# Kernel tuning notes

Measured on AMD Instinct MI355X. Metric: run time of the kernel, lower is better.

## Reference

```python
import jax, jax.numpy as jnp
import numpy as np

D = 384      # d_model
DM = 256     # memory feature dim
DF = 1536    # dim_feedforward
EPS = 1e-5


def _layer_norm(x, g, b):
    m = jnp.mean(x, axis=-1, keepdims=True)
    v = jnp.mean(jnp.square(x - m), axis=-1, keepdims=True)
    return (x - m) * jax.lax.rsqrt(v + EPS) * g + b


def setup_inputs() -> dict:
    key = jax.random.key(0)
    ks = jax.random.split(key, 24)
    B, T, T1, Tc = 8, 2048, 2048, 2048
    s = 0.02
    inp = {
        "tgt": jax.random.normal(ks[0], (B, T, D), jnp.float32),
        "memory": jax.random.normal(ks[1], (B, T1, DM), jnp.float32),
        "a1": jnp.float32(0.5),
        "score_c": jax.random.normal(ks[2], (B, 1, Tc, T1), jnp.float32) * 0.1,
        "out_c": jax.random.normal(ks[3], (B, Tc, D), jnp.float32),
        # attention projections
        "Wq": jax.random.normal(ks[4], (D, D), jnp.float32) * s,
        "bq": jnp.zeros((D,), jnp.float32),
        "Wk": jax.random.normal(ks[5], (DM, D), jnp.float32) * s,
        "bk": jnp.zeros((D,), jnp.float32),
        "Wv": jax.random.normal(ks[6], (DM, D), jnp.float32) * s,
        "bv": jnp.zeros((D,), jnp.float32),
        "Wu": jax.random.normal(ks[7], (D, D), jnp.float32) * s,  # unknown
        "bu": jnp.zeros((D,), jnp.float32),
        "Wn": jax.random.normal(ks[8], (D, D), jnp.float32) * s,  # known
        "bn": jnp.zeros((D,), jnp.float32),
        # FFN
        "W1": jax.random.normal(ks[9], (D, DF), jnp.float32) * s,
        "b1": jnp.zeros((DF,), jnp.float32),
        "W2": jax.random.normal(ks[10], (DF, D), jnp.float32) * s,
        "b2": jnp.zeros((D,), jnp.float32),
        # LayerNorms
        "g1": jnp.ones((D,), jnp.float32),
        "be1": jnp.zeros((D,), jnp.float32),
        "g2": jnp.ones((D,), jnp.float32),
        "be2": jnp.zeros((D,), jnp.float32),
    }
    return inp


def reference(tgt, memory, a1, score_c, out_c,
              Wq, bq, Wk, bk, Wv, bv, Wu, bu, Wn, bn,
              W1, b1, W2, b2, g1, be1, g2, be2):
    # --- En_De_Attention (n_head = 1; dropout p=0 / eval mode -> identity) ---
    scale = 1.0 / jnp.sqrt(jnp.float32(D))
    q = tgt @ Wq + bq                  # [B,T,D]
    k = memory @ Wk + bk               # [B,T1,D]
    v = memory @ Wv + bv               # [B,T1,D]
    att = jnp.einsum('btd,bsd->bts', q, k) * scale            # [B,T,T1]

    unknow = tgt @ Wu + bu             # [B,T,D]
    know = out_c @ Wn + bn             # [B,Tc,D]
    score1 = jnp.einsum('btd,bcd->btc', unknow, know) * scale  # [B,T,Tc]
    mixed = jnp.einsum('btc,bcs->bts', score1, score_c[:, 0])  # [B,T,T1]

    # tt = a1 in (0,1]: blended-score branch of the original module
    score = a1 * jax.nn.softmax(mixed, axis=-1) \
          + (1.0 - a1) * jax.nn.softmax(att, axis=-1)          # [B,T,T1]
    z = jnp.einsum('bts,bsd->btd', score, v)                   # [B,T,D]

    # --- residual + norm1 ---
    x = _layer_norm(tgt + z, g1, be1)
    # --- FFN (relu) + residual + norm2 (dropout eval -> identity) ---
    ff = jax.nn.relu(x @ W1 + b1) @ W2 + b2
    out = _layer_norm(x + ff, g2, be2)
    # score2 returned with head dim, matching torch shape [B,1,T,T1]
    return out, score[:, None]
```

## Files before the change

kernel.cpp:

```cpp
#include <hip/hip_runtime.h>
#include <stdint.h>

typedef __attribute__((ext_vector_type(8))) short bf16x8;
typedef __attribute__((ext_vector_type(4))) float f32x4;

__device__ __forceinline__ short f2bf(float f) {
    union { float f; unsigned u; } v; v.f = f;
    unsigned r = v.u + 0x7fffu + ((v.u >> 16) & 1u);
    return (short)(r >> 16);
}
__device__ __forceinline__ float bf2f(short s) {
    union { unsigned u; float f; } v;
    v.u = ((unsigned)(unsigned short)s) << 16;
    return v.f;
}

__device__ __forceinline__ void gld16(const void* g, void* l) {
    auto gp = reinterpret_cast<const __attribute__((address_space(1))) unsigned int*>(
        reinterpret_cast<uintptr_t>(g));
    auto lp = reinterpret_cast<__attribute__((address_space(3))) unsigned int*>(
        reinterpret_cast<uintptr_t>(l));
    __builtin_amdgcn_global_load_lds(gp, lp, 16, 0, 0);
}

template<int OUTBF, int BIASMODE , int DORELU>
__global__ __launch_bounds__(256, 2) void gemmWide(
    const short* __restrict__ Ag, const short* __restrict__ Bg,
    void* __restrict__ Cg, const float* __restrict__ bias,
    int K, int lda, int ldb, int ldc,
    long long sA, long long sB, long long sC,
    long long dA, long long dB, long long dC, float scale)
{
    __shared__ short lds[3 * 12288];
    const int t = threadIdx.x;
    const int lane = t & 63;
    const int wave = t >> 6;
    const int wm = wave >> 1, wn = wave & 1;

    const int gx = gridDim.x, gy = gridDim.y;
    const int nwg = gx * gy * gridDim.z;
    int id = blockIdx.x + gx * (blockIdx.y + gy * blockIdx.z);
    id = (id & 7) * (nwg >> 3) + (id >> 3);
    const int bx = id % gx;
    const int by = (id / gx) % gy;
    const int bz = id / (gx * gy);
    const int zlo = bz & 7, zhi = bz >> 3;

    const long long row0 = (long long)by * 128;
    const long long col0 = (long long)bx * 256;
    const int NT = K >> 5;

    const int gk = ((t & 3) ^ ((t >> 2) & 3) ^ ((t >> 4) & 3)) * 8;
    const short* Asrc = Ag + zlo * sA + zhi * dA + (row0 + (t >> 2)) * (long long)lda + gk;
    const short* Bsrc = Bg + zlo * sB + zhi * dB + (col0 + (t >> 2)) * (long long)ldb + gk;

    const int frow = lane & 15;
    const int fcol = ((lane >> 4) ^ (frow & 3) ^ ((frow >> 2) & 3)) * 8;

    f32x4 acc[4][8] = {};

#define STG(BUF, KC) do { \
        gld16(Asrc + (KC), &lds[(BUF) * 12288 + t * 8]); \
        gld16(Asrc + (KC) + 64LL * lda, &lds[(BUF) * 12288 + 2048 + t * 8]); \
        gld16(Bsrc + (KC), &lds[(BUF) * 12288 + 4096 + t * 8]); \
        gld16(Bsrc + (KC) + 64LL * ldb, &lds[(BUF) * 12288 + 6144 + t * 8]); \
        gld16(Bsrc + (KC) + 128LL * ldb, &lds[(BUF) * 12288 + 8192 + t * 8]); \
        gld16(Bsrc + (KC) + 192LL * ldb, &lds[(BUF) * 12288 + 10240 + t * 8]); } while (0)

    STG(0, 0);
    STG(1, 32);
    asm volatile("s_waitcnt vmcnt(6)\ns_barrier" ::: "memory");

    for (int kt = 0; kt < NT; ++kt) {
        const int rb = (kt % 3) * 12288;
        bf16x8 av[4], bv[8];
#pragma unroll
        for (int m = 0; m < 4; ++m)
            av[m] = *(const bf16x8*)&lds[rb + (wm * 64 + m * 16 + frow) * 32 + fcol];
#pragma unroll
        for (int n = 0; n < 8; ++n)
            bv[n] = *(const bf16x8*)&lds[rb + 4096 + (wn * 128 + n * 16 + frow) * 32 + fcol];
        if (kt + 2 < NT) STG((kt + 2) % 3, (long long)(kt + 2) * 32);
        __builtin_amdgcn_s_setprio(1);
#pragma unroll
        for (int m = 0; m < 4; ++m)
#pragma unroll
            for (int n = 0; n < 8; ++n)
                acc[m][n] = __builtin_amdgcn_mfma_f32_16x16x32_bf16(av[m], bv[n], acc[m][n], 0, 0, 0);
        __builtin_amdgcn_s_setprio(0);
        if (kt + 1 < NT) {
            if (kt + 2 < NT) asm volatile("s_waitcnt vmcnt(6)\ns_barrier" ::: "memory");
            else             asm volatile("s_waitcnt vmcnt(0)\ns_barrier" ::: "memory");
        }
    }
#undef STG

    const int crow = (lane >> 4) * 4;
    const int ccol = lane & 15;
    const long long cz = zlo * sC + zhi * dC;
#pragma unroll
    for (int m = 0; m < 4; ++m)
#pragma unroll
        for (int n = 0; n < 8; ++n)
#pragma unroll
            for (int i = 0; i < 4; ++i) {
                long long r = row0 + wm * 64 + m * 16 + crow + i;
                long long c = col0 + wn * 128 + n * 16 + ccol;
                float v = acc[m][n][i] * scale;
                if (BIASMODE == 1) v += bias[c];
                if (DORELU) v = fmaxf(v, 0.0f);
                long long idx = cz + r * (long long)ldc + c;
                if (OUTBF) ((short*)Cg)[idx] = f2bf(v);
                else ((float*)Cg)[idx] = v;
            }
}

template<int OUTBF, int BIASMODE , int DORELU>
__global__ __launch_bounds__(256, 3) void gemm128r(
    const short* __restrict__ Ag, const short* __restrict__ Bg,
    void* __restrict__ Cg, const float* __restrict__ bias,
    int K, int lda, int ldb, int ldc,
    long long sA, long long sB, long long sC,
    long long dA, long long dB, long long dC, float scale)
{
    __shared__ short lds[3 * 8192];
    const int t = threadIdx.x;
    const int lane = t & 63;
    const int wave = t >> 6;
    const int wm = wave >> 1, wn = wave & 1;

    const int gx = gridDim.x, gy = gridDim.y;
    const int nwg = gx * gy * gridDim.z;
    int id = blockIdx.x + gx * (blockIdx.y + gy * blockIdx.z);
    id = (id & 7) * (nwg >> 3) + (id >> 3);
    const int bx = id % gx;
    const int by = (id / gx) % gy;
    const int bz = id / (gx * gy);
    const int zlo = bz & 7, zhi = bz >> 3;

    const long long row0 = (long long)by * 128;
    const long long col0 = (long long)bx * 128;
    const int NT = K >> 5;

    const int gk = ((t & 3) ^ ((t >> 2) & 3) ^ ((t >> 4) & 3)) * 8;
    const short* Asrc = Ag + zlo * sA + zhi * dA + (row0 + (t >> 2)) * (long long)lda + gk;
    const short* Bsrc = Bg + zlo * sB + zhi * dB + (col0 + (t >> 2)) * (long long)ldb + gk;

    const int frow = lane & 15;
    const int fcol = ((lane >> 4) ^ (frow & 3) ^ ((frow >> 2) & 3)) * 8;

    f32x4 acc[4][4] = {};

#define STG(BUF, KC) do { \
        gld16(Asrc + (KC), &lds[(BUF) * 8192 + t * 8]); \
        gld16(Asrc + (KC) + 64LL * lda, &lds[(BUF) * 8192 + 2048 + t * 8]); \
        gld16(Bsrc + (KC), &lds[(BUF) * 8192 + 4096 + t * 8]); \
        gld16(Bsrc + (KC) + 64LL * ldb, &lds[(BUF) * 8192 + 6144 + t * 8]); } while (0)

    STG(0, 0);
    STG(1, 32);
    asm volatile("s_waitcnt vmcnt(4)\ns_barrier" ::: "memory");

    for (int kt = 0; kt < NT; ++kt) {
        const int rb = (kt % 3) * 8192;
        bf16x8 av[4], bv[4];
#pragma unroll
        for (int m = 0; m < 4; ++m)
            av[m] = *(const bf16x8*)&lds[rb + (wm * 64 + m * 16 + frow) * 32 + fcol];
#pragma unroll
        for (int n = 0; n < 4; ++n)
            bv[n] = *(const bf16x8*)&lds[rb + 4096 + (wn * 64 + n * 16 + frow) * 32 + fcol];
        if (kt + 2 < NT) STG((kt + 2) % 3, (long long)(kt + 2) * 32);
        __builtin_amdgcn_s_setprio(1);
#pragma unroll
        for (int m = 0; m < 4; ++m)
#pragma unroll
            for (int n = 0; n < 4; ++n)
                acc[m][n] = __builtin_amdgcn_mfma_f32_16x16x32_bf16(av[m], bv[n], acc[m][n], 0, 0, 0);
        __builtin_amdgcn_s_setprio(0);
        if (kt + 1 < NT) {
            if (kt + 2 < NT) asm volatile("s_waitcnt vmcnt(4)\ns_barrier" ::: "memory");
            else             asm volatile("s_waitcnt vmcnt(0)\ns_barrier" ::: "memory");
        }
    }
#undef STG

    const int crow = (lane >> 4) * 4;
    const int ccol = lane & 15;
    const long long cz = zlo * sC + zhi * dC;
#pragma unroll
    for (int m = 0; m < 4; ++m)
#pragma unroll
        for (int n = 0; n < 4; ++n)
#pragma unroll
            for (int i = 0; i < 4; ++i) {
                long long r = row0 + wm * 64 + m * 16 + crow + i;
                long long c = col0 + wn * 64 + n * 16 + ccol;
                float v = acc[m][n][i] * scale;
                if (BIASMODE == 1) v += bias[c];
                if (BIASMODE == 2) v += bias[r];
                if (DORELU) v = fmaxf(v, 0.0f);
                long long idx = cz + r * (long long)ldc + c;
                if (OUTBF) ((short*)Cg)[idx] = f2bf(v);
                else ((float*)Cg)[idx] = v;
            }
}

__global__ __launch_bounds__(256, 3) void gemm128rr(
    const short* __restrict__ A1, const short* __restrict__ B1,
    short* __restrict__ C1, const float* __restrict__ bias1,
    int K1, int lda1, int ldb1, int ldc1,
    const short* __restrict__ A2, const short* __restrict__ B2,
    short* __restrict__ C2, const float* __restrict__ bias2,
    int K2, int lda2, int ldb2, int ldc2)
{
    __shared__ short lds[3 * 8192];
    const int t = threadIdx.x;
    const int lane = t & 63;
    const int wave = t >> 6;
    const int wm = wave >> 1, wn = wave & 1;

    const int gx = gridDim.x, gy = gridDim.y;
    const int nwg = gx * gy;
    int id = blockIdx.x + gx * blockIdx.y;
    id = (id & 7) * (nwg >> 3) + (id >> 3);
    const int bx = id % gx;
    const int by = id / gx;

    const bool sel = bx >= 6;
    const int bxx = sel ? bx - 6 : bx;
    const short* Ag = sel ? A2 : A1;
    const short* Bg = sel ? B2 : B1;
    short* Cg = sel ? C2 : C1;
    const float* bias = sel ? bias2 : bias1;
    const int K = sel ? K2 : K1;
    const int lda = sel ? lda2 : lda1;
    const int ldb = sel ? ldb2 : ldb1;
    const int ldc = sel ? ldc2 : ldc1;

    const long long row0 = (long long)by * 128;
    const long long col0 = (long long)bxx * 128;
    const int NT = K >> 5;

    const int gk = ((t & 3) ^ ((t >> 2) & 3) ^ ((t >> 4) & 3)) * 8;
    const short* Asrc = Ag + (row0 + (t >> 2)) * (long long)lda + gk;
    const short* Bsrc = Bg + (col0 + (t >> 2)) * (long long)ldb + gk;

    const int frow = lane & 15;
    const int fcol = ((lane >> 4) ^ (frow & 3) ^ ((frow >> 2) & 3)) * 8;

    f32x4 acc[4][4] = {};

#define STG(BUF, KC) do { \
        gld16(Asrc + (KC), &lds[(BUF) * 8192 + t * 8]); \
        gld16(Asrc + (KC) + 64LL * lda, &lds[(BUF) * 8192 + 2048 + t * 8]); \
        gld16(Bsrc + (KC), &lds[(BUF) * 8192 + 4096 + t * 8]); \
        gld16(Bsrc + (KC) + 64LL * ldb, &lds[(BUF) * 8192 + 6144 + t * 8]); } while (0)

    STG(0, 0);
    STG(1, 32);
    asm volatile("s_waitcnt vmcnt(4)\ns_barrier" ::: "memory");

    for (int kt = 0; kt < NT; ++kt) {
        const int rb = (kt % 3) * 8192;
        bf16x8 av[4], bv[4];
#pragma unroll
        for (int m = 0; m < 4; ++m)
            av[m] = *(const bf16x8*)&lds[rb + (wm * 64 + m * 16 + frow) * 32 + fcol];
#pragma unroll
        for (int n = 0; n < 4; ++n)
            bv[n] = *(const bf16x8*)&lds[rb + 4096 + (wn * 64 + n * 16 + frow) * 32 + fcol];
        if (kt + 2 < NT) STG((kt + 2) % 3, (long long)(kt + 2) * 32);
        __builtin_amdgcn_s_setprio(1);
#pragma unroll
        for (int m = 0; m < 4; ++m)
#pragma unroll
            for (int n = 0; n < 4; ++n)
                acc[m][n] = __builtin_amdgcn_mfma_f32_16x16x32_bf16(av[m], bv[n], acc[m][n], 0, 0, 0);
        __builtin_amdgcn_s_setprio(0);
        if (kt + 1 < NT) {
            if (kt + 2 < NT) asm volatile("s_waitcnt vmcnt(4)\ns_barrier" ::: "memory");
            else             asm volatile("s_waitcnt vmcnt(0)\ns_barrier" ::: "memory");
        }
    }
#undef STG

    const int crow = (lane >> 4) * 4;
    const int ccol = lane & 15;
#pragma unroll
    for (int m = 0; m < 4; ++m)
#pragma unroll
        for (int n = 0; n < 4; ++n)
#pragma unroll
            for (int i = 0; i < 4; ++i) {
                long long r = row0 + wm * 64 + m * 16 + crow + i;
                long long c = col0 + wn * 64 + n * 16 + ccol;
                float v = acc[m][n][i] + bias[c];
                Cg[r * (long long)ldc + c] = f2bf(v);
            }
}

#define RD_A(RB, M, KS) (*(const bf16x8*)&lds[(RB) + (wm * 64 + (M) * 16 + frow) * 64 + \
        ((((KS) << 2) | fq) ^ (frow & 7)) * 8])
#define RD_B(RB, Nn, KS) (*(const bf16x8*)&lds[(RB) + 8192 + (wn * 64 + (Nn) * 16 + frow) * 64 + \
        ((((KS) << 2) | fq) ^ (frow & 7)) * 8])

__global__ __launch_bounds__(256, 2) void gemm128pz(
    const short* __restrict__ A1, const short* __restrict__ B1, short* __restrict__ C1,
    const float* __restrict__ bias1, int K1, int lda1, int ldb1, int ldc1,
    long long sB1, long long sC1,
    const short* __restrict__ A2, const short* __restrict__ B2, short* __restrict__ C2,
    const float* __restrict__ bias2, int K2, int lda2, int ldb2, int ldc2,
    long long sB2, long long sC2)
{
    __shared__ short lds[2 * 16384];
    const int t = threadIdx.x;
    const int lane = t & 63;
    const int wave = t >> 6;
    const int wm = wave >> 1, wn = wave & 1;

    const int gx = gridDim.x, gy = gridDim.y;
    const int nwg = gx * gy * gridDim.z;
    int id = blockIdx.x + gx * (blockIdx.y + gy * blockIdx.z);
    id = (id & 7) * (nwg >> 3) + (id >> 3);
    const int bx = id % gx;
    const int by = (id / gx) % gy;
    const int bz = id / (gx * gy);

    const bool sel = bz >= 8;
    const int zz = bz & 7;
    const short* Ag = sel ? A2 : A1;
    const short* Bg = sel ? B2 : B1;
    short* Cg = sel ? C2 : C1;
    const float* bias = sel ? bias2 : bias1;
    const int K = sel ? K2 : K1;
    const int lda = sel ? lda2 : lda1;
    const int ldb = sel ? ldb2 : ldb1;
    const int ldc = sel ? ldc2 : ldc1;
    const long long sB = sel ? sB2 : sB1;
    const long long sC = sel ? sC2 : sC1;

    const long long row0 = (long long)by * 128;
    const long long col0 = (long long)bx * 128;
    const int NT = K >> 6;

    const int srow = t >> 3;
    const int gk = ((t & 7) ^ (srow & 7)) * 8;
    const short* Asrc = Ag + (row0 + srow) * (long long)lda + gk;
    const short* Bsrc = Bg + (long long)zz * sB + (col0 + srow) * (long long)ldb + gk;

    const int frow = lane & 15;
    const int fq = lane >> 4;

    f32x4 acc[4][4] = {};

#define STAGE_A(WB, KC) do { _Pragma("unroll") \
        for (int r = 0; r < 4; ++r) \
            gld16(Asrc + (KC) + (long long)r * 32 * lda, &lds[(WB) + t * 8 + r * 2048]); } while (0)
#define STAGE_B(WB, KC) do { _Pragma("unroll") \
        for (int r = 0; r < 4; ++r) \
            gld16(Bsrc + (KC) + (long long)r * 32 * ldb, &lds[(WB) + 8192 + t * 8 + r * 2048]); } while (0)

    STAGE_A(0, 0);
    STAGE_B(0, 0);
    asm volatile("s_waitcnt vmcnt(0)\ns_barrier" ::: "memory");

    for (int kt = 0; kt < NT; ++kt) {
        const int rb = (kt & 1) << 14;
        const int wb = ((kt + 1) & 1) << 14;
        const bool st = (kt + 1) < NT;
        const long long kc = (long long)(kt + 1) << 6;

        bf16x8 av[4], bv[4];

#pragma unroll
        for (int m = 0; m < 4; ++m) av[m] = RD_A(rb, m, 0);
#pragma unroll
        for (int n = 0; n < 4; ++n) bv[n] = RD_B(rb, n, 0);
        if (st) STAGE_A(wb, kc);
        asm volatile("s_barrier" ::: "memory");
        __builtin_amdgcn_s_setprio(1);
#pragma unroll
        for (int m = 0; m < 4; ++m)
#pragma unroll
            for (int n = 0; n < 4; ++n)
                acc[m][n] = __builtin_amdgcn_mfma_f32_16x16x32_bf16(av[m], bv[n], acc[m][n], 0, 0, 0);
        __builtin_amdgcn_s_setprio(0);
        asm volatile("s_barrier" ::: "memory");

#pragma unroll
        for (int m = 0; m < 4; ++m) av[m] = RD_A(rb, m, 1);
#pragma unroll
        for (int n = 0; n < 4; ++n) bv[n] = RD_B(rb, n, 1);
        if (st) STAGE_B(wb, kc);
        asm volatile("s_barrier" ::: "memory");
        __builtin_amdgcn_s_setprio(1);
#pragma unroll
        for (int m = 0; m < 4; ++m)
#pragma unroll
            for (int n = 0; n < 4; ++n)
                acc[m][n] = __builtin_amdgcn_mfma_f32_16x16x32_bf16(av[m], bv[n], acc[m][n], 0, 0, 0);
        __builtin_amdgcn_s_setprio(0);
        if (st) asm volatile("s_waitcnt vmcnt(0)\ns_barrier" ::: "memory");
        else    asm volatile("s_barrier" ::: "memory");
    }
#undef STAGE_A
#undef STAGE_B

    const int crow = (lane >> 4) * 4;
    const int ccol = lane & 15;
    const long long cz = (long long)zz * sC;
#pragma unroll
    for (int m = 0; m < 4; ++m)
#pragma unroll
        for (int n = 0; n < 4; ++n)
#pragma unroll
            for (int i = 0; i < 4; ++i) {
                long long r = row0 + wm * 64 + m * 16 + crow + i;
                long long c = col0 + wn * 64 + n * 16 + ccol;
                float v = acc[m][n][i] + bias[r];
                Cg[cz + r * (long long)ldc + c] = f2bf(v);
            }
}
#undef RD_A
#undef RD_B

__global__ __launch_bounds__(256) void prologue(
    const float* __restrict__ tgt, const float* __restrict__ mem, const float* __restrict__ outc,
    const float* __restrict__ bq, const float* __restrict__ bu,
    short* __restrict__ tgtb, short* __restrict__ memb, short* __restrict__ outcb,
    float* __restrict__ qubias,
    const float* __restrict__ Wq, const float* __restrict__ Wk, const float* __restrict__ Wv,
    const float* __restrict__ Wu, const float* __restrict__ Wn,
    const float* __restrict__ W1, const float* __restrict__ W2,
    short* __restrict__ WquT, short* __restrict__ WkT, short* __restrict__ WvT,
    short* __restrict__ WnT, short* __restrict__ W1T, short* __restrict__ W2T,
    const float* __restrict__ score_c, short* __restrict__ scoreCt)
{
    __shared__ __align__(16) char smem[33792];
    const int blk = blockIdx.x;
    const int t = threadIdx.x;

    if (blk < 4096) {
        const long long R1 = 1572864;
        const long long R2 = R1 + 1048576;
        const long long base = (long long)blk * 1024 + t;
#pragma unroll
        for (int s = 0; s < 4; ++s) {
            long long i = base + s * 256;
            const float* in; short* out; long long j;
            if (i < R1) { in = tgt; out = tgtb; j = i; }
            else if (i < R2) { in = mem; out = memb; j = i - R1; }
            else { in = outc; out = outcb; j = i - R2; }
            float4 v = ((const float4*)in)[j];
            short4 o;
            o.x = f2bf(v.x); o.y = f2bf(v.y); o.z = f2bf(v.z); o.w = f2bf(v.w);
            ((short4*)out)[j] = o;
        }
        return;
    }

    if (blk == 4096) {
        if (t < 192)
            ((float4*)qubias)[t] = (t < 96) ? ((const float4*)bq)[t] : ((const float4*)bu)[t - 96];
        return;
    }

    if (blk < 4541) {
        float (*tile)[65] = (float(*)[65])smem;
        int b = blk - 4097;
        const float* in; short* out; int R, C, local;
        if (b < 36)       { in = Wq; out = WquT;          R = 384;  C = 384;  local = b; }
        else if (b < 60)  { in = Wk; out = WkT;           R = 256;  C = 384;  local = b - 36; }
        else if (b < 84)  { in = Wv; out = WvT;           R = 256;  C = 384;  local = b - 60; }
        else if (b < 120) { in = Wu; out = WquT + 147456; R = 384;  C = 384;  local = b - 84; }
        else if (b < 156) { in = Wn; out = WnT;           R = 384;  C = 384;  local = b - 120; }
        else if (b < 300) { in = W1; out = W1T;           R = 384;  C = 1536; local = b - 156; }
        else              { in = W2; out = W2T;           R = 1536; C = 384;  local = b - 300; }
        const int nbx = C >> 6;
        const int r0 = (local / nbx) * 64, c0 = (local % nbx) * 64;
        const int lr = t >> 6, lc = t & 63;
#pragma unroll
        for (int i = 0; i < 16; ++i) {
            int r = lr * 16 + i;
            tile[r][lc] = in[(long long)(r0 + r) * C + c0 + lc];
        }
        __syncthreads();
#pragma unroll
        for (int i = 0; i < 16; ++i) {
            int r = lr * 16 + i;
            out[(long long)(c0 + r) * R + r0 + lc] = f2bf(tile[lc][r]);
        }
        return;
    }

    {
        short (*stile)[264] = (short(*)[264])smem;
        const long long S2 = 2048LL * 2048;
        int local = blk - 4541;
        const int ct = local & 7;
        const int rt = (local >> 3) & 31;
        const int bz = local >> 8;
        const long long zoff = (long long)bz * S2;
        const int r0 = rt * 64, c0 = ct * 256;

        const int tr = t >> 2;
        const int tc = t & 3;
        const float* src = score_c + zoff + (long long)(r0 + tr) * 2048 + c0 + tc * 64;
#pragma unroll
        for (int i = 0; i < 16; ++i) {
            float4 v = ((const float4*)src)[i];
            short4 o;
            o.x = f2bf(v.x); o.y = f2bf(v.y); o.z = f2bf(v.z); o.w = f2bf(v.w);
            *(short4*)&stile[tr][tc * 64 + i * 4] = o;
        }
        __syncthreads();
        short* dst = scoreCt + zoff + (long long)(c0 + t) * 2048 + r0;
#pragma unroll
        for (int rr = 0; rr < 16; ++rr) {
            short4 o;
            o.x = stile[4 * rr + 0][t];
            o.y = stile[4 * rr + 1][t];
            o.z = stile[4 * rr + 2][t];
            o.w = stile[4 * rr + 3][t];
            ((short4*)dst)[rr] = o;
        }
    }
}

__global__ __launch_bounds__(256) void softmax_blend(
    const short* __restrict__ attb, const short* __restrict__ mixb,
    const float* __restrict__ a1p,
    float* __restrict__ outF, short* __restrict__ outB)
{
    const int S = 2048;
    const long long row = blockIdx.x;
    const short* ar = attb + row * S;
    const short* mr = mixb + row * S;
    const int t = threadIdx.x;
    const int wave = t >> 6;

    bf16x8 a8 = *(const bf16x8*)&ar[t * 8];
    bf16x8 m8 = *(const bf16x8*)&mr[t * 8];
    float av[8], mv[8];
#pragma unroll
    for (int i = 0; i < 8; ++i) { av[i] = bf2f(a8[i]); mv[i] = bf2f(m8[i]); }

    float amax = av[0], mmax = mv[0];
#pragma unroll
    for (int i = 1; i < 8; ++i) { amax = fmaxf(amax, av[i]); mmax = fmaxf(mmax, mv[i]); }
#pragma unroll
    for (int o = 32; o; o >>= 1) {
        amax = fmaxf(amax, __shfl_xor(amax, o));
        mmax = fmaxf(mmax, __shfl_xor(mmax, o));
    }
    __shared__ float red[2][4];
    if ((t & 63) == 0) { red[0][wave] = amax; red[1][wave] = mmax; }
    __syncthreads();
    amax = fmaxf(fmaxf(red[0][0], red[0][1]), fmaxf(red[0][2], red[0][3]));
    mmax = fmaxf(fmaxf(red[1][0], red[1][1]), fmaxf(red[1][2], red[1][3]));

    float asum = 0.f, msum = 0.f;
#pragma unroll
    for (int i = 0; i < 8; ++i) {
        av[i] = __expf(av[i] - amax); asum += av[i];
        mv[i] = __expf(mv[i] - mmax); msum += mv[i];
    }
#pragma unroll
    for (int o = 32; o; o >>= 1) {
        asum += __shfl_xor(asum, o);
        msum += __shfl_xor(msum, o);
    }
    __shared__ float red2[2][4];
    if ((t & 63) == 0) { red2[0][wave] = asum; red2[1][wave] = msum; }
    __syncthreads();
    asum = red2[0][0] + red2[0][1] + red2[0][2] + red2[0][3];
    msum = red2[1][0] + red2[1][1] + red2[1][2] + red2[1][3];

    const float a1 = a1p[0];
    const float wm = a1 / msum;
    const float wa = (1.0f - a1) / asum;

    float o0[8];
    bf16x8 ob;
#pragma unroll
    for (int i = 0; i < 8; ++i) {
        float s = wm * mv[i] + wa * av[i];
        o0[i] = s;
        ob[i] = f2bf(s);
    }
    float4 f0, f1;
    f0.x = o0[0]; f0.y = o0[1]; f0.z = o0[2]; f0.w = o0[3];
    f1.x = o0[4]; f1.y = o0[5]; f1.z = o0[6]; f1.w = o0[7];
    *(float4*)&outF[row * S + t * 8] = f0;
    *(float4*)&outF[row * S + t * 8 + 4] = f1;
    *(bf16x8*)&outB[row * S + t * 8] = ob;
}

template<int WRITE_F, int WRITE_BF, int TWO_Y, int XBF>
__global__ __launch_bounds__(256) void ln_kernel(
    const void* __restrict__ Xv, const float* __restrict__ Yr,
    const float* __restrict__ Y2,
    const float* __restrict__ g, const float* __restrict__ be,
    float* __restrict__ outF, short* __restrict__ outB)
{
    const int Dm = 384;
    const int wave = threadIdx.x >> 6, lane = threadIdx.x & 63;
    const long long row = (long long)blockIdx.x * 4 + wave;
    const float* y = Yr + row * Dm;
    const float* y2 = TWO_Y ? (Y2 + row * Dm) : nullptr;
    float h[6];
    float s = 0.f, s2 = 0.f;
#pragma unroll
    for (int j = 0; j < 6; ++j) {
        int c = j * 64 + lane;
        float xv;
        if (XBF) xv = bf2f(((const short*)Xv)[row * Dm + c]);
        else     xv = ((const float*)Xv)[row * Dm + c];
        h[j] = xv + y[c];
        if (TWO_Y) h[j] += y2[c];
        s += h[j]; s2 += h[j] * h[j];
    }
#pragma unroll
    for (int o = 32; o; o >>= 1) { s += __shfl_xor(s, o); s2 += __shfl_xor(s2, o); }
    const float mean = s * (1.0f / 384.0f);
    const float var = s2 * (1.0f / 384.0f) - mean * mean;
    const float rstd = rsqrtf(var + 1e-5f);
#pragma unroll
    for (int j = 0; j < 6; ++j) {
        int c = j * 64 + lane;
        float v = (h[j] - mean) * rstd * g[c] + be[c];
        if (WRITE_F) outF[row * Dm + c] = v;
        if (WRITE_BF) outB[row * Dm + c] = f2bf(v);
    }
}

extern "C" void kernel_launch(void* const* d_in, const int* in_sizes, int n_in,
                              void* d_out, int out_size, void* d_ws, size_t ws_size,
                              hipStream_t stream) {
    const float* tgt     = (const float*)d_in[0];
    const float* memory  = (const float*)d_in[1];
    const float* a1      = (const float*)d_in[2];
    const float* score_c = (const float*)d_in[3];
    const float* out_c   = (const float*)d_in[4];
    const float* Wq = (const float*)d_in[5];  const float* bq = (const float*)d_in[6];
    const float* Wk = (const float*)d_in[7];  const float* bk = (const float*)d_in[8];
    const float* Wv = (const float*)d_in[9];  const float* bv = (const float*)d_in[10];
    const float* Wu = (const float*)d_in[11]; const float* bu = (const float*)d_in[12];
    const float* Wn = (const float*)d_in[13]; const float* bn = (const float*)d_in[14];
    const float* W1 = (const float*)d_in[15]; const float* b1 = (const float*)d_in[16];
    const float* W2 = (const float*)d_in[17]; const float* b2 = (const float*)d_in[18];
    const float* g1 = (const float*)d_in[19]; const float* be1 = (const float*)d_in[20];
    const float* g2 = (const float*)d_in[21]; const float* be2 = (const float*)d_in[22];

    const long long BT = 16384;
    const long long S2 = 2048LL * 2048;
    const long long PB = 2048LL * 384;
    char* ws = (char*)d_ws;
    size_t off = 0;
    auto A_ = [&](size_t b) { size_t r = off; off += (b + 255) & ~(size_t)255; return r; };

    const size_t oTgtB  = A_(BT * 384 * 2);
    const size_t oMemB  = A_(BT * 256 * 2);
    const size_t oOutcB = A_(BT * 384 * 2);
    const size_t oWquT  = A_(768 * 384 * 2);
    const size_t oWnT   = A_(384 * 384 * 2);
    const size_t oWkT   = A_(384 * 256 * 2);
    const size_t oWvT   = A_(384 * 256 * 2);
    const size_t oW1T   = A_(1536 * 384 * 2);
    const size_t oW2T   = A_(384 * 1536 * 2);
    const size_t oQUb   = A_(768 * 4);
    const size_t oQU    = A_(16 * PB * 2);
    const size_t oKP    = A_(16 * PB * 2);
    const size_t oVT    = A_(8LL * 384 * 2048 * 2);
    const size_t oJ     = A_(8 * S2 * 2);
    const size_t oKr    = A_(8 * S2 * 2);
    const size_t oAM    = A_(16 * S2 * 2);
    const size_t oXB    = A_(BT * 384 * 2);

    short* tgt_bf  = (short*)(ws + oTgtB);
    short* mem_bf  = (short*)(ws + oMemB);
    short* outc_bf = (short*)(ws + oOutcB);
    short* WquT = (short*)(ws + oWquT);
    short* WnT  = (short*)(ws + oWnT);
    short* WkT  = (short*)(ws + oWkT);
    short* WvT  = (short*)(ws + oWvT);
    short* W1T  = (short*)(ws + oW1T);
    short* W2T  = (short*)(ws + oW2T);
    float* qu_bias = (float*)(ws + oQUb);
    short* qu_bf  = (short*)(ws + oQU);
    short* k_bf   = (short*)(ws + oKP);
    short* Pt_bf  = k_bf + 8 * PB;
    short* vT_bf  = (short*)(ws + oVT);
    short* score_bf = (short*)(ws + oJ);
    short* scoreCt  = (short*)(ws + oKr);
    float* z0_f     = (float*)(ws + oKr);
    float* z1_f     = z0_f + 6291456;
    short* knoT_bf  = (short*)(ws + oAM);
    short* att_bf   = (short*)(ws + oAM);
    short* mix_bf   = att_bf + 8 * S2;
    short* h_bf     = (short*)(ws + oAM);
    float* ff_f     = (float*)(ws + oAM + 8 * S2 * 2);
    short* x_bf = (short*)(ws + oXB);

    float* outMain = (float*)d_out;
    float* outScore = (float*)d_out + 6291456;

    const float SC = 0.05103103630798288f;
    dim3 blk(256);

    prologue<<<6589, blk, 0, stream>>>(
        tgt, memory, out_c, bq, bu, tgt_bf, mem_bf, outc_bf, qu_bias,
        Wq, Wk, Wv, Wu, Wn, W1, W2, WquT, WkT, WvT, WnT, W1T, W2T,
        score_c, scoreCt);

    gemm128rr<<<dim3(9, 128, 1), blk, 0, stream>>>(
        tgt_bf, WquT, qu_bf, qu_bias, 384, 384, 384, 768,
        mem_bf, WkT, k_bf, bk, 256, 256, 256, 384);
    gemm128pz<<<dim3(16, 3, 16), blk, 0, stream>>>(
        WvT, mem_bf, vT_bf, bv, 256, 256, 256, 2048, 2048LL * 256, PB,
        WnT, outc_bf, knoT_bf, bn, 384, 384, 384, 2048, PB, PB);
    gemm128r<1, 0, 0><<<dim3(3, 16, 8), blk, 0, stream>>>(
        scoreCt, knoT_bf, Pt_bf, nullptr, 2048, 2048, 2048, 384,
        S2, PB, PB, 0, 0, 0, 1.0f);
    gemmWide<1, 0, 0><<<dim3(8, 16, 16), blk, 0, stream>>>(
        qu_bf, k_bf, att_bf, nullptr, 384, 768, 384, 2048,
        2048LL * 768, PB, S2, 384, 8 * PB, 8 * S2, SC);
    softmax_blend<<<16384, blk, 0, stream>>>(att_bf, mix_bf, a1, outScore, score_bf);
    gemm128r<0, 0, 0><<<dim3(3, 16, 16), blk, 0, stream>>>(
        score_bf, vT_bf, z0_f, nullptr, 1024, 2048, 2048, 384,
        S2, PB, PB, 1024, 1024, 6291456, 1.0f);
    ln_kernel<0, 1, 1, 0><<<4096, blk, 0, stream>>>(
        tgt, z0_f, z1_f, g1, be1, nullptr, x_bf);
    gemm128r<1, 1, 1><<<dim3(12, 128, 1), blk, 0, stream>>>(
        x_bf, W1T, h_bf, b1, 384, 384, 384, 1536, 0, 0, 0, 0, 0, 0, 1.0f);
    gemm128r<0, 1, 0><<<dim3(3, 128, 1), blk, 0, stream>>>(
        h_bf, W2T, ff_f, b2, 1536, 1536, 1536, 384, 0, 0, 0, 0, 0, 0, 1.0f);
    ln_kernel<1, 0, 0, 1><<<4096, blk, 0, stream>>>(
        x_bf, ff_f, nullptr, g2, be2, outMain, nullptr);
}
```

Baseline: 431.8 us.

## Fuse score_c transpose and bf16 cast into a dedicated TN GEMM

The prologue no longer converts and transposes score_c into a bf16 scratch copy. A new gemmTN kernel reads fp32 score_c directly in its original layout, converts it to bf16 in registers and writes it into swizzled LDS for the MFMA. The aim is to drop a full 8x2048x2048 write and re-read pass through global memory. In exchange, A-operand loads are register-staged fp32 loads instead of async LDS loads, which may expose latency inside the GEMM loop.

After: 428.2 us. About the same (-0.8%).

```diff
diff --git a/kernel.cpp b/kernel.cpp
--- a/kernel.cpp
+++ b/kernel.cpp
@@ -2,6 +2,7 @@
 #include <stdint.h>
 
 typedef __attribute__((ext_vector_type(8))) short bf16x8;
+typedef __attribute__((ext_vector_type(4))) short bf16x4;
 typedef __attribute__((ext_vector_type(4))) float f32x4;
 
 __device__ __forceinline__ short f2bf(float f) {
@@ -21,6 +22,111 @@
     auto lp = reinterpret_cast<__attribute__((address_space(3))) unsigned int*>(
         reinterpret_cast<uintptr_t>(l));
     __builtin_amdgcn_global_load_lds(gp, lp, 16, 0, 0);
+}
+
+__global__ __launch_bounds__(256, 3) void gemmTN(
+    const float* __restrict__ Ag, const short* __restrict__ Bg,
+    short* __restrict__ Cg,
+    long long sA, long long sB, long long sC)
+{
+    __shared__ short lds[2 * 8256];
+    const int t = threadIdx.x;
+    const int lane = t & 63;
+    const int wave = t >> 6;
+    const int wm = wave >> 1, wn = wave & 1;
+
+    const int nwg = 3 * 16 * 8;
+    int id = blockIdx.x + 3 * (blockIdx.y + 16 * blockIdx.z);
+    id = (id & 7) * (nwg >> 3) + (id >> 3);
+    const int bx = id % 3;
+    const int by = (id / 3) % 16;
+    const int bz = id / 48;
+
+    const long long s0 = (long long)by * 128;
+    const int d0 = bx * 128;
+    const int q = t >> 5, kk = t & 31;
+    const float* Asrc = Ag + bz * sA + (long long)(q * 4) * 2048 + s0 + kk * 4;
+
+    const int gk = ((t & 3) ^ ((t >> 2) & 3) ^ ((t >> 4) & 3)) * 8;
+    const short* Bsrc = Bg + bz * sB + (d0 + (t >> 2)) * 2048LL + gk;
+
+    const int frow = lane & 15;
+    const int g = lane >> 4;
+    const int fcol = (g ^ (frow & 3) ^ ((frow >> 2) & 3)) * 8;
+
+    f32x4 acc[4][4] = {};
+    f32x4 ar[4];
+
+#define STAGE_B(BUF, KC) do { \
+        gld16(Bsrc + (KC), &lds[(BUF) + 4160 + t * 8]); \
+        gld16(Bsrc + (KC) + 64LL * 2048, &lds[(BUF) + 4160 + 2048 + t * 8]); } while (0)
+
+#define WRITE_A(BUF) do { \
+        short tmp[16]; \
+        _Pragma("unroll") \
+        for (int i = 0; i < 16; ++i) tmp[i] = f2bf(ar[i & 3][i >> 2]); \
+        short* dst = &lds[(BUF) + q * 520 + kk * 16]; \
+        *(bf16x8*)dst = *(bf16x8*)&tmp[0]; \
+        *(bf16x8*)(dst + 8) = *(bf16x8*)&tmp[8]; } while (0)
+
+#pragma unroll
+    for (int r = 0; r < 4; ++r) ar[r] = *(const f32x4*)&Asrc[(long long)r * 2048];
+    STAGE_B(0, 0);
+    WRITE_A(0);
+    asm volatile("s_waitcnt vmcnt(0) lgkmcnt(0)\ns_barrier" ::: "memory");
+#pragma unroll
+    for (int r = 0; r < 4; ++r) ar[r] = *(const f32x4*)&Asrc[65536LL + r * 2048];
+
+    const int NT = 64;
+    for (int kt = 0; kt < NT; ++kt) {
+        const int rb = (kt & 1) * 8256;
+        const int wb = ((kt + 1) & 1) * 8256;
+
+        bf16x8 av[4], bv[4];
+#pragma unroll
+        for (int m = 0; m < 4; ++m) {
+            const int sl = (wm * 64 + m * 16 + frow) * 4;
+            bf16x4 lo = *(const bf16x4*)&lds[rb + 1040 * g + sl];
+            bf16x4 hi = *(const bf16x4*)&lds[rb + 1040 * g + 520 + sl];
+            av[m] = __builtin_shufflevector(lo, hi, 0, 1, 2, 3, 4, 5, 6, 7);
+        }
+#pragma unroll
+        for (int n = 0; n < 4; ++n)
+            bv[n] = *(const bf16x8*)&lds[rb + 4160 + (wn * 64 + n * 16 + frow) * 32 + fcol];
+
+        if (kt + 1 < NT) {
+            STAGE_B(wb, (long long)(kt + 1) * 32);
+            WRITE_A(wb);
+        }
+#pragma unroll
+        for (int m = 0; m < 4; ++m)
+#pragma unroll
+            for (int n = 0; n < 4; ++n)
+                acc[m][n] = __builtin_amdgcn_mfma_f32_16x16x32_bf16(av[m], bv[n], acc[m][n], 0, 0, 0);
+        if (kt + 1 < NT) {
+            asm volatile("s_waitcnt vmcnt(0) lgkmcnt(0)\ns_barrier" ::: "memory");
+            if (kt + 2 < NT) {
+#pragma unroll
+                for (int r = 0; r < 4; ++r)
+                    ar[r] = *(const f32x4*)&Asrc[(long long)(kt + 2) * 65536 + r * 2048];
+            }
+        }
+    }
+#undef STAGE_B
+#undef WRITE_A
+
+    const int crow = (lane >> 4) * 4;
+    const int ccol = lane & 15;
+#pragma unroll
+    for (int m = 0; m < 4; ++m)
+#pragma unroll
+        for (int n = 0; n < 4; ++n)
+#pragma unroll
+            for (int i = 0; i < 4; ++i) {
+                long long r = s0 + wm * 64 + m * 16 + crow + i;
+                long long c = d0 + wn * 64 + n * 16 + ccol;
+                Cg[bz * sC + r * 384 + c] = f2bf(acc[m][n][i]);
+            }
 }
 
 template<int OUTBF, int BIASMODE , int DORELU>
@@ -434,10 +540,9 @@
     const float* __restrict__ Wu, const float* __restrict__ Wn,
     const float* __restrict__ W1, const float* __restrict__ W2,
     short* __restrict__ WquT, short* __restrict__ WkT, short* __restrict__ WvT,
-    short* __restrict__ WnT, short* __restrict__ W1T, short* __restrict__ W2T,
-    const float* __restrict__ score_c, short* __restrict__ scoreCt)
+    short* __restrict__ WnT, short* __restrict__ W1T, short* __restrict__ W2T)
 {
-    __shared__ __align__(16) char smem[33792];
+    __shared__ float tile[64][65];
     const int blk = blockIdx.x;
     const int t = threadIdx.x;
 
@@ -466,65 +571,28 @@
         return;
     }
 
-    if (blk < 4541) {
-        float (*tile)[65] = (float(*)[65])smem;
-        int b = blk - 4097;
-        const float* in; short* out; int R, C, local;
-        if (b < 36)       { in = Wq; out = WquT;          R = 384;  C = 384;  local = b; }
-        else if (b < 60)  { in = Wk; out = WkT;           R = 256;  C = 384;  local = b - 36; }
-        else if (b < 84)  { in = Wv; out = WvT;           R = 256;  C = 384;  local = b - 60; }
-        else if (b < 120) { in = Wu; out = WquT + 147456; R = 384;  C = 384;  local = b - 84; }
-        else if (b < 156) { in = Wn; out = WnT;           R = 384;  C = 384;  local = b - 120; }
-        else if (b < 300) { in = W1; out = W1T;           R = 384;  C = 1536; local = b - 156; }
-        else              { in = W2; out = W2T;           R = 1536; C = 384;  local = b - 300; }
-        const int nbx = C >> 6;
-        const int r0 = (local / nbx) * 64, c0 = (local % nbx) * 64;
-        const int lr = t >> 6, lc = t & 63;
-#pragma unroll
-        for (int i = 0; i < 16; ++i) {
-            int r = lr * 16 + i;
-            tile[r][lc] = in[(long long)(r0 + r) * C + c0 + lc];
-        }
-        __syncthreads();
-#pragma unroll
-        for (int i = 0; i < 16; ++i) {
-            int r = lr * 16 + i;
-            out[(long long)(c0 + r) * R + r0 + lc] = f2bf(tile[lc][r]);
-        }
-        return;
-    }
-
-    {
-        short (*stile)[264] = (short(*)[264])smem;
-        const long long S2 = 2048LL * 2048;
-        int local = blk - 4541;
-        const int ct = local & 7;
-        const int rt = (local >> 3) & 31;
-        const int bz = local >> 8;
-        const long long zoff = (long long)bz * S2;
-        const int r0 = rt * 64, c0 = ct * 256;
-
-        const int tr = t >> 2;
-        const int tc = t & 3;
-        const float* src = score_c + zoff + (long long)(r0 + tr) * 2048 + c0 + tc * 64;
-#pragma unroll
-        for (int i = 0; i < 16; ++i) {
-            float4 v = ((const float4*)src)[i];
-            short4 o;
-            o.x = f2bf(v.x); o.y = f2bf(v.y); o.z = f2bf(v.z); o.w = f2bf(v.w);
-            *(short4*)&stile[tr][tc * 64 + i * 4] = o;
-        }
-        __syncthreads();
-        short* dst = scoreCt + zoff + (long long)(c0 + t) * 2048 + r0;
-#pragma unroll
-        for (int rr = 0; rr < 16; ++rr) {
-            short4 o;
-            o.x = stile[4 * rr + 0][t];
-            o.y = stile[4 * rr + 1][t];
-            o.z = stile[4 * rr + 2][t];
-            o.w = stile[4 * rr + 3][t];
-            ((short4*)dst)[rr] = o;
-        }
+    int b = blk - 4097;
+    const float* in; short* out; int R, C, local;
+    if (b < 36)       { in = Wq; out = WquT;          R = 384;  C = 384;  local = b; }
+    else if (b < 60)  { in = Wk; out = WkT;           R = 256;  C = 384;  local = b - 36; }
+    else if (b < 84)  { in = Wv; out = WvT;           R = 256;  C = 384;  local = b - 60; }
+    else if (b < 120) { in = Wu; out = WquT + 147456; R = 384;  C = 384;  local = b - 84; }
+    else if (b < 156) { in = Wn; out = WnT;           R = 384;  C = 384;  local = b - 120; }
+    else if (b < 300) { in = W1; out = W1T;           R = 384;  C = 1536; local = b - 156; }
+    else              { in = W2; out = W2T;           R = 1536; C = 384;  local = b - 300; }
+    const int nbx = C >> 6;
+    const int r0 = (local / nbx) * 64, c0 = (local % nbx) * 64;
+    const int lr = t >> 6, lc = t & 63;
+#pragma unroll
+    for (int i = 0; i < 16; ++i) {
+        int r = lr * 16 + i;
+        tile[r][lc] = in[(long long)(r0 + r) * C + c0 + lc];
+    }
+    __syncthreads();
+#pragma unroll
+    for (int i = 0; i < 16; ++i) {
+        int r = lr * 16 + i;
+        out[(long long)(c0 + r) * R + r0 + lc] = f2bf(tile[lc][r]);
     }
 }
 
@@ -693,7 +761,6 @@
     short* Pt_bf  = k_bf + 8 * PB;
     short* vT_bf  = (short*)(ws + oVT);
     short* score_bf = (short*)(ws + oJ);
-    short* scoreCt  = (short*)(ws + oKr);
     float* z0_f     = (float*)(ws + oKr);
     float* z1_f     = z0_f + 6291456;
     short* knoT_bf  = (short*)(ws + oAM);
@@ -709,10 +776,9 @@
     const float SC = 0.05103103630798288f;
     dim3 blk(256);
 
-    prologue<<<6589, blk, 0, stream>>>(
+    prologue<<<4541, blk, 0, stream>>>(
         tgt, memory, out_c, bq, bu, tgt_bf, mem_bf, outc_bf, qu_bias,
-        Wq, Wk, Wv, Wu, Wn, W1, W2, WquT, WkT, WvT, WnT, W1T, W2T,
-        score_c, scoreCt);
+        Wq, Wk, Wv, Wu, Wn, W1, W2, WquT, WkT, WvT, WnT, W1T, W2T);
 
     gemm128rr<<<dim3(9, 128, 1), blk, 0, stream>>>(
         tgt_bf, WquT, qu_bf, qu_bias, 384, 384, 384, 768,
@@ -720,9 +786,8 @@
     gemm128pz<<<dim3(16, 3, 16), blk, 0, stream>>>(
         WvT, mem_bf, vT_bf, bv, 256, 256, 256, 2048, 2048LL * 256, PB,
         WnT, outc_bf, knoT_bf, bn, 384, 384, 384, 2048, PB, PB);
-    gemm128r<1, 0, 0><<<dim3(3, 16, 8), blk, 0, stream>>>(
-        scoreCt, knoT_bf, Pt_bf, nullptr, 2048, 2048, 2048, 384,
-        S2, PB, PB, 0, 0, 0, 1.0f);
+    gemmTN<<<dim3(3, 16, 8), blk, 0, stream>>>(
+        score_c, knoT_bf, Pt_bf, S2, PB, PB);
     gemmWide<1, 0, 0><<<dim3(8, 16, 16), blk, 0, stream>>>(
         qu_bf, k_bf, att_bf, nullptr, 384, 768, 384, 2048,
         2048LL * 768, PB, S2, 384, 8 * PB, 8 * S2, SC);
```
